# Optimization experiments

Hardware: AMD Instinct MI355X
Metric: run time of the kernel (lower is better)

Reference implementation:

```python
import jax, jax.numpy as jnp
import numpy as np

N_NODES = 100000
N_EDGES = 1600000
D_IN, D_HID, D_OUT = 128, 128, 64


def setup_inputs() -> dict:
    key = jax.random.key(0)
    ks = jax.random.split(key, 8)
    x = jax.random.normal(ks[0], (N_NODES, D_IN), dtype=jnp.float32)
    edge_index = jax.random.randint(ks[1], (2, N_EDGES), 0, N_NODES, dtype=jnp.int64)
    def glorot(k, fan_in, fan_out):
        s = jnp.sqrt(6.0 / (fan_in + fan_out))
        return jax.random.uniform(k, (fan_in, fan_out), jnp.float32, -s, s)
    return {
        "x": x,
        "edge_index": edge_index,
        "W1": glorot(ks[2], D_IN, D_HID), "b1": jnp.zeros((D_HID,), jnp.float32),
        "W2": glorot(ks[3], D_HID, D_HID), "b2": jnp.zeros((D_HID,), jnp.float32),
        "W3": glorot(ks[4], D_HID, D_OUT), "b3": jnp.zeros((D_OUT,), jnp.float32),
    }


def _gcn_norm(edge_index, n_nodes):
    # add self-loops, compute symmetric normalization D^-1/2 A D^-1/2
    loop = jnp.arange(n_nodes, dtype=edge_index.dtype)
    src = jnp.concatenate([edge_index[0], loop])  # message source
    dst = jnp.concatenate([edge_index[1], loop])  # aggregation target
    deg = jax.ops.segment_sum(jnp.ones_like(dst, dtype=jnp.float32), dst,
                              num_segments=n_nodes)
    dinv = jnp.where(deg > 0, jax.lax.rsqrt(deg), 0.0)
    norm = dinv[src] * dinv[dst]  # [E + N]
    return src, dst, norm


def _gcn_conv(x, W, b, src, dst, norm, n_nodes):
    xw = x @ W                                # dense transform [N, F_out]
    msg = xw[src] * norm[:, None]             # gather + scale   [E+N, F_out]
    out = jax.ops.segment_sum(msg, dst, num_segments=n_nodes)  # scatter-add
    return out + b


def reference(x, edge_index, W1, b1, W2, b2, W3, b3):
    n = x.shape[0]
    src, dst, norm = _gcn_norm(edge_index, n)  # cached=True: same norm reused
    h = jax.nn.relu(_gcn_conv(x, W1, b1, src, dst, norm, n))
    h = jax.nn.relu(_gcn_conv(h, W2, b2, src, dst, norm, n))
    return _gcn_conv(h, W3, b3, src, dst, norm, n)
```

## Files before the change

kernel.cpp:

```cpp
#include <hip/hip_runtime.h>
#include <hip/hip_fp16.h>


#define NN 100000
#define NE 1600000
#define TT (NE + NN)
#define BSH 9
#define NBUCK ((NN + 511) / 512)
#define EPB1 2048
#define NPB1 ((TT + EPB1 - 1) / EPB1)

typedef _Float16 f16x8 __attribute__((ext_vector_type(8)));
typedef float f32x4 __attribute__((ext_vector_type(4)));


__global__ __launch_bounds__(256) void wt_conv_all(const float* __restrict__ W1,
                                                   const float* __restrict__ W2,
                                                   const float* __restrict__ W3,
                                                   _Float16* __restrict__ Wt1,
                                                   _Float16* __restrict__ Wt2,
                                                   _Float16* __restrict__ Wt3,
                                                   int* __restrict__ gbc,
                                                   int* __restrict__ done,
                                                   int* __restrict__ bbase,
                                                   int* __restrict__ rowptr) {
    int idx = blockIdx.x * 256 + threadIdx.x;
    if (idx < 16384) {
        Wt1[(idx % 128) * 128 + idx / 128] = (_Float16)W1[idx];
    } else if (idx < 32768) {
        int i = idx - 16384;
        Wt2[(i % 128) * 128 + i / 128] = (_Float16)W2[i];
    } else if (idx < 40960) {
        int i = idx - 32768;
        Wt3[(i % 64) * 128 + i / 64] = (_Float16)W3[i];
    }
    if (idx < NBUCK) gbc[idx] = 0;
    if (idx == 0) { *done = 0; bbase[NBUCK] = TT; rowptr[NN] = TT; }
}


__global__ __launch_bounds__(256) void bucket_count(const int* __restrict__ ei,
                                                    int* __restrict__ gbc,
                                                    int* __restrict__ done,
                                                    int* __restrict__ bbase,
                                                    int* __restrict__ gcursor) {
    __shared__ int hist[NBUCK];
    __shared__ int amlast;
    const int tid = threadIdx.x;
    const int base = blockIdx.x * EPB1;
    for (int b = tid; b < NBUCK; b += 256) hist[b] = 0;
    __syncthreads();
    for (int i = tid; i < EPB1; i += 256) {
        int e = base + i;
        if (e >= TT) break;
        int d = (e < NE) ? ei[NE + e] : (e - NE);
        atomicAdd(&hist[d >> BSH], 1);
    }
    __syncthreads();
    for (int b = tid; b < NBUCK; b += 256)
        if (hist[b]) atomicAdd(&gbc[b], hist[b]);
    __threadfence();
    if (tid == 0) amlast = (atomicAdd(done, 1) == (int)gridDim.x - 1);
    __syncthreads();
    if (amlast) {
        __threadfence();
        __shared__ int s[256];
        int v = (tid < NBUCK)
            ? __hip_atomic_load(&gbc[tid], __ATOMIC_RELAXED,
                                __HIP_MEMORY_SCOPE_AGENT) : 0;
        s[tid] = v;
        __syncthreads();
        for (int off = 1; off < 256; off <<= 1) {
            int u = (tid >= off) ? s[tid - off] : 0;
            __syncthreads();
            s[tid] += u;
            __syncthreads();
        }
        if (tid < NBUCK) {
            int excl = s[tid] - v;
            bbase[tid] = excl;
            gcursor[tid] = excl;
        }
    }
}


__global__ __launch_bounds__(256) void partition_p1(const int* __restrict__ ei,
                                                    int* __restrict__ gcursor,
                                                    int* __restrict__ part) {
    __shared__ int hist[NBUCK];
    const int tid = threadIdx.x;
    const int base = blockIdx.x * EPB1;
    for (int b = tid; b < NBUCK; b += 256) hist[b] = 0;
    __syncthreads();
    for (int i = tid; i < EPB1; i += 256) {
        int e = base + i;
        if (e >= TT) break;
        int d = (e < NE) ? ei[NE + e] : (e - NE);
        atomicAdd(&hist[d >> BSH], 1);
    }
    __syncthreads();
    for (int b = tid; b < NBUCK; b += 256) {
        int cnt = hist[b];
        hist[b] = cnt ? atomicAdd(&gcursor[b], cnt) : 0;
    }
    __syncthreads();
    for (int i = tid; i < EPB1; i += 256) {
        int e = base + i;
        if (e >= TT) break;
        int s, d;
        if (e < NE) { s = ei[e]; d = ei[NE + e]; }
        else        { s = d = e - NE; }
        int pos = atomicAdd(&hist[d >> BSH], 1);
        part[pos] = s | ((d & 511) << 17);
    }
}


__global__ __launch_bounds__(512) void partition_p2(const int* __restrict__ part,
                                                    const int* __restrict__ bbase,
                                                    int* __restrict__ rowptr,
                                                    float* __restrict__ dinv,
                                                    int* __restrict__ col) {
    __shared__ int cnt[512];
    __shared__ int scn[512];
    __shared__ int cur[512];
    const int b = blockIdx.x;
    const int v0 = b << BSH;
    const int nv = min(512, NN - v0);
    const int tid = threadIdx.x;
    const int base = bbase[b];
    const int nrec = bbase[b + 1] - base;

    cnt[tid] = 0;
    __syncthreads();
    for (int i = tid; i < nrec; i += 512)
        atomicAdd(&cnt[((unsigned)part[base + i]) >> 17], 1);
    __syncthreads();
    scn[tid] = cnt[tid];
    __syncthreads();
    for (int off = 1; off < 512; off <<= 1) {
        int a = (tid >= off) ? scn[tid - off] : 0;
        __syncthreads();
        scn[tid] += a;
        __syncthreads();
    }
    if (tid < nv) {
        int excl = scn[tid] - cnt[tid];
        rowptr[v0 + tid] = base + excl;
        dinv[v0 + tid] = rsqrtf((float)cnt[tid]);
        cur[tid] = base + excl;
    }
    __syncthreads();
    for (int i = tid; i < nrec; i += 512) {
        int r = part[base + i];
        int pos = atomicAdd(&cur[((unsigned)r) >> 17], 1);
        col[pos] = r & 0x1FFFF;
    }
}


template <int F, bool AHALF>
__global__ __launch_bounds__(256) void gemm_mfma(const void* __restrict__ Ap,
                                                 const _Float16* __restrict__ Wt,
                                                 const float* __restrict__ dinv,
                                                 __half* __restrict__ Yh) {
    constexpr int NT = F / 16;
    __shared__ _Float16 Yl[64][136];

    const int tid = threadIdx.x;
    const int wave = tid >> 6;
    const int lane = tid & 63;
    const int m = lane & 15;
    const int q = lane >> 4;
    const int grow0 = blockIdx.x * 64;
    const int row = grow0 + wave * 16 + m;
    const bool rok = row < NN;

    f32x4 acc[NT];
#pragma unroll
    for (int t = 0; t < NT; t++) acc[t] = (f32x4){0.f, 0.f, 0.f, 0.f};

#pragma unroll
    for (int kt = 0; kt < 128; kt += 32) {
        const int k0 = kt + q * 8;
        union { f16x8 v; _Float16 e[8]; } au;
        if (rok) {
            if constexpr (AHALF) {
                au.v = *reinterpret_cast<const f16x8*>(
                    (const __half*)Ap + (size_t)row * 128 + k0);
            } else {
                const float* A = (const float*)Ap;
                float4 x0 = *reinterpret_cast<const float4*>(A + (size_t)row * 128 + k0);
                float4 x1 = *reinterpret_cast<const float4*>(A + (size_t)row * 128 + k0 + 4);
                au.e[0] = (_Float16)x0.x; au.e[1] = (_Float16)x0.y;
                au.e[2] = (_Float16)x0.z; au.e[3] = (_Float16)x0.w;
                au.e[4] = (_Float16)x1.x; au.e[5] = (_Float16)x1.y;
                au.e[6] = (_Float16)x1.z; au.e[7] = (_Float16)x1.w;
            }
        } else {
#pragma unroll
            for (int j = 0; j < 8; j++) au.e[j] = (_Float16)0.f;
        }
#pragma unroll
        for (int t = 0; t < NT; t++) {
            f16x8 bf = *reinterpret_cast<const f16x8*>(Wt + (t * 16 + m) * 128 + k0);
            acc[t] = __builtin_amdgcn_mfma_f32_16x16x32_f16(au.v, bf, acc[t], 0, 0, 0);
        }
    }
#pragma unroll
    for (int r = 0; r < 4; r++) {
        int lrow = wave * 16 + q * 4 + r;
        int gr = grow0 + lrow;
        float s = (gr < NN) ? dinv[gr] : 0.f;
#pragma unroll
        for (int t = 0; t < NT; t++)
            Yl[lrow][t * 16 + m] = (_Float16)(s * acc[t][r]);
    }
    __syncthreads();
    constexpr int CH = F / 8;
    for (int i = tid; i < 64 * CH; i += 256) {
        int lrow = i / CH, c = i % CH;
        int gr = grow0 + lrow;
        if (gr < NN)
            *reinterpret_cast<f16x8*>(Yh + (size_t)gr * F + c * 8) =
                *reinterpret_cast<const f16x8*>(&Yl[lrow][c * 8]);
    }
}


__device__ __forceinline__ void acc_add8(float* acc, float4 raw) {
    const __half2* h2 = reinterpret_cast<const __half2*>(&raw);
#pragma unroll
    for (int qq = 0; qq < 4; qq++) {
        float2 fv = __half22float2(h2[qq]);
        acc[2 * qq]     += fv.x;
        acc[2 * qq + 1] += fv.y;
    }
}


template <int FOUT>
__global__ __launch_bounds__(256) void fused_agg_gemm(
        const __half* __restrict__ XWh,
        const int* __restrict__ rowptr,
        const int* __restrict__ col,
        const float* __restrict__ dinv,
        const float* __restrict__ bias,
        const _Float16* __restrict__ Wt,
        __half* __restrict__ Yout) {
    __shared__ _Float16 Hs[16][136];
    __shared__ _Float16 Ds[16][FOUT + 8];

    const int tid = threadIdx.x;
    const int v0 = blockIdx.x * 16;

    {
        const int lnode = tid >> 4;
        const int f = tid & 15;
        const int v = v0 + lnode;
        const int beg = rowptr[v];
        const int end = rowptr[v + 1];
        const float4* base = reinterpret_cast<const float4*>(XWh);
        float acc[8] = {0.f, 0.f, 0.f, 0.f, 0.f, 0.f, 0.f, 0.f};
#pragma unroll 4
        for (int e = beg; e < end; e++) {
            int u = col[e];
            float4 raw = base[(size_t)u * 16 + f];
            acc_add8(acc, raw);
        }
        const float dv = dinv[v];
        union { f16x8 v8; _Float16 e8[8]; } hu;
#pragma unroll
        for (int qq = 0; qq < 8; qq++) {
            float r = dv * acc[qq] + bias[f * 8 + qq];
            hu.e8[qq] = (_Float16)fmaxf(r, 0.f);
        }
        *reinterpret_cast<f16x8*>(&Hs[lnode][f * 8]) = hu.v8;
    }
    __syncthreads();

    constexpr int TPW = FOUT / 64;
    const int wave = tid >> 6;
    const int lane = tid & 63;
    const int m = lane & 15;
    const int q = lane >> 4;
    f32x4 gacc[TPW];
#pragma unroll
    for (int t = 0; t < TPW; t++) gacc[t] = (f32x4){0.f, 0.f, 0.f, 0.f};
#pragma unroll
    for (int kt = 0; kt < 128; kt += 32) {
        const int k0 = kt + q * 8;
        f16x8 av = *reinterpret_cast<const f16x8*>(&Hs[m][k0]);
#pragma unroll
        for (int t = 0; t < TPW; t++) {
            const int gc = (wave * TPW + t) * 16 + m;
            f16x8 bv = *reinterpret_cast<const f16x8*>(Wt + gc * 128 + k0);
            gacc[t] = __builtin_amdgcn_mfma_f32_16x16x32_f16(av, bv, gacc[t], 0, 0, 0);
        }
    }
#pragma unroll
    for (int r = 0; r < 4; r++) {
        const int lrow = q * 4 + r;
        const float s = dinv[v0 + lrow];
#pragma unroll
        for (int t = 0; t < TPW; t++)
            Ds[lrow][(wave * TPW + t) * 16 + m] = (_Float16)(s * gacc[t][r]);
    }
    __syncthreads();
    constexpr int CH = FOUT / 8;
    for (int i2 = tid; i2 < 16 * CH; i2 += 256) {
        int lrow = i2 / CH, c = i2 % CH;
        *reinterpret_cast<f16x8*>(Yout + (size_t)(v0 + lrow) * FOUT + c * 8) =
            *reinterpret_cast<const f16x8*>(&Ds[lrow][c * 8]);
    }
}


__global__ __launch_bounds__(256) void agg_final(
        const __half* __restrict__ XWh,
        const int* __restrict__ rowptr,
        const int* __restrict__ col,
        const float* __restrict__ dinv,
        const float* __restrict__ bias,
        float* __restrict__ out) {
    constexpr int TPN = 8;
    constexpr int NPB = 256 / TPN;
    const int v = blockIdx.x * NPB + threadIdx.x / TPN;
    const int f = threadIdx.x % TPN;
    const int beg = rowptr[v];
    const int end = rowptr[v + 1];
    const float4* base = reinterpret_cast<const float4*>(XWh);
    float acc[8] = {0.f, 0.f, 0.f, 0.f, 0.f, 0.f, 0.f, 0.f};
#pragma unroll 4
    for (int e = beg; e < end; e++) {
        int u = col[e];
        float4 raw = base[(size_t)u * TPN + f];
        acc_add8(acc, raw);
    }
    const float dv = dinv[v];
    float r[8];
#pragma unroll
    for (int q = 0; q < 8; q++)
        r[q] = dv * acc[q] + bias[f * 8 + q];
    float* op = out + (size_t)v * 64 + f * 8;
    *reinterpret_cast<float4*>(op)     = make_float4(r[0], r[1], r[2], r[3]);
    *reinterpret_cast<float4*>(op + 4) = make_float4(r[4], r[5], r[6], r[7]);
}


extern "C" void kernel_launch(void* const* d_in, const int* in_sizes, int n_in,
                              void* d_out, int out_size, void* d_ws, size_t ws_size,
                              hipStream_t stream) {
    const float* x  = (const float*)d_in[0];
    const int*   ei = (const int*)d_in[1];
    const float* W1 = (const float*)d_in[2];
    const float* b1 = (const float*)d_in[3];
    const float* W2 = (const float*)d_in[4];
    const float* b2 = (const float*)d_in[5];
    const float* W3 = (const float*)d_in[6];
    const float* b3 = (const float*)d_in[7];
    float* out = (float*)d_out;

    char* p = (char*)d_ws;
    int*      rowptr  = (int*)p;       p += 400016;
    float*    dinv    = (float*)p;     p += 400000;
    int*      gbc     = (int*)p;       p += 1024;
    int*      bbase   = (int*)p;       p += 1024;
    int*      gcursor = (int*)p;       p += 1024;
    int*      done    = (int*)p;       p += 1024;
    _Float16* Wt1     = (_Float16*)p;  p += 32768;
    _Float16* Wt2     = (_Float16*)p;  p += 32768;
    _Float16* Wt3     = (_Float16*)p;  p += 16384;
    int*      part    = (int*)p;       p += (size_t)TT * 4;
    int*      col     = (int*)p;       p += (size_t)TT * 4;
    __half*   xwh1    = (__half*)p;    p += (size_t)NN * 128 * 2;
    __half*   xwh2    = (__half*)p;
    __half*   xwh3    = xwh1;

    wt_conv_all<<<160, 256, 0, stream>>>(W1, W2, W3, Wt1, Wt2, Wt3,
                                         gbc, done, bbase, rowptr);
    bucket_count<<<NPB1, 256, 0, stream>>>(ei, gbc, done, bbase, gcursor);
    partition_p1<<<NPB1, 256, 0, stream>>>(ei, gcursor, part);
    partition_p2<<<NBUCK, 512, 0, stream>>>(part, bbase, rowptr, dinv, col);

    const int gb = (NN + 63) / 64;
    const int fb = NN / 16;
    gemm_mfma<128, false><<<gb, 256, 0, stream>>>(x, Wt1, dinv, xwh1);
    fused_agg_gemm<128><<<fb, 256, 0, stream>>>(xwh1, rowptr, col, dinv, b1,
                                                Wt2, xwh2);
    fused_agg_gemm<64><<<fb, 256, 0, stream>>>(xwh2, rowptr, col, dinv, b2,
                                               Wt3, xwh3);
    agg_final<<<NN / 32, 256, 0, stream>>>(xwh3, rowptr, col, dinv, b3, out);
}
```

Baseline: 471.4 us.

## Drop bucket-count pass by partitioning into fixed-capacity bucket slots

```diff
diff --git a/kernel.cpp b/kernel.cpp
--- a/kernel.cpp
+++ b/kernel.cpp
@@ -7,8 +7,9 @@
 #define TT (NE + NN)
 #define BSH 9
 #define NBUCK ((NN + 511) / 512)
-#define EPB1 2048
+#define EPB1 8192
 #define NPB1 ((TT + EPB1 - 1) / EPB1)
+#define SLOT 12288
 
 typedef _Float16 f16x8 __attribute__((ext_vector_type(8)));
 typedef float f32x4 __attribute__((ext_vector_type(4)));
@@ -20,9 +21,7 @@
                                                    _Float16* __restrict__ Wt1,
                                                    _Float16* __restrict__ Wt2,
                                                    _Float16* __restrict__ Wt3,
-                                                   int* __restrict__ gbc,
-                                                   int* __restrict__ done,
-                                                   int* __restrict__ bbase,
+                                                   int* __restrict__ gcursor,
                                                    int* __restrict__ rowptr) {
     int idx = blockIdx.x * 256 + threadIdx.x;
     if (idx < 16384) {
@@ -34,109 +33,74 @@
         int i = idx - 32768;
         Wt3[(i % 64) * 128 + i / 64] = (_Float16)W3[i];
     }
-    if (idx < NBUCK) gbc[idx] = 0;
-    if (idx == 0) { *done = 0; bbase[NBUCK] = TT; rowptr[NN] = TT; }
-}
-
-
-__global__ __launch_bounds__(256) void bucket_count(const int* __restrict__ ei,
-                                                    int* __restrict__ gbc,
-                                                    int* __restrict__ done,
-                                                    int* __restrict__ bbase,
-                                                    int* __restrict__ gcursor) {
+    if (idx < NBUCK) gcursor[idx] = 0;
+    if (idx == 0) rowptr[NN] = TT;
+}
+
+
+__global__ __launch_bounds__(1024) void partition_p1(const int* __restrict__ ei,
+                                                     int* __restrict__ gcursor,
+                                                     int* __restrict__ part) {
     __shared__ int hist[NBUCK];
-    __shared__ int amlast;
     const int tid = threadIdx.x;
     const int base = blockIdx.x * EPB1;
-    for (int b = tid; b < NBUCK; b += 256) hist[b] = 0;
-    __syncthreads();
-    for (int i = tid; i < EPB1; i += 256) {
+    for (int b = tid; b < NBUCK; b += 1024) hist[b] = 0;
+    __syncthreads();
+    for (int i = tid; i < EPB1; i += 1024) {
         int e = base + i;
         if (e >= TT) break;
         int d = (e < NE) ? ei[NE + e] : (e - NE);
         atomicAdd(&hist[d >> BSH], 1);
     }
     __syncthreads();
-    for (int b = tid; b < NBUCK; b += 256)
-        if (hist[b]) atomicAdd(&gbc[b], hist[b]);
-    __threadfence();
-    if (tid == 0) amlast = (atomicAdd(done, 1) == (int)gridDim.x - 1);
-    __syncthreads();
-    if (amlast) {
-        __threadfence();
-        __shared__ int s[256];
-        int v = (tid < NBUCK)
-            ? __hip_atomic_load(&gbc[tid], __ATOMIC_RELAXED,
-                                __HIP_MEMORY_SCOPE_AGENT) : 0;
-        s[tid] = v;
-        __syncthreads();
-        for (int off = 1; off < 256; off <<= 1) {
-            int u = (tid >= off) ? s[tid - off] : 0;
-            __syncthreads();
-            s[tid] += u;
-            __syncthreads();
-        }
-        if (tid < NBUCK) {
-            int excl = s[tid] - v;
-            bbase[tid] = excl;
-            gcursor[tid] = excl;
-        }
-    }
-}
-
-
-__global__ __launch_bounds__(256) void partition_p1(const int* __restrict__ ei,
-                                                    int* __restrict__ gcursor,
-                                                    int* __restrict__ part) {
-    __shared__ int hist[NBUCK];
-    const int tid = threadIdx.x;
-    const int base = blockIdx.x * EPB1;
-    for (int b = tid; b < NBUCK; b += 256) hist[b] = 0;
-    __syncthreads();
-    for (int i = tid; i < EPB1; i += 256) {
-        int e = base + i;
-        if (e >= TT) break;
-        int d = (e < NE) ? ei[NE + e] : (e - NE);
-        atomicAdd(&hist[d >> BSH], 1);
-    }
-    __syncthreads();
-    for (int b = tid; b < NBUCK; b += 256) {
+    for (int b = tid; b < NBUCK; b += 1024) {
         int cnt = hist[b];
         hist[b] = cnt ? atomicAdd(&gcursor[b], cnt) : 0;
     }
     __syncthreads();
-    for (int i = tid; i < EPB1; i += 256) {
+    for (int i = tid; i < EPB1; i += 1024) {
         int e = base + i;
         if (e >= TT) break;
         int s, d;
         if (e < NE) { s = ei[e]; d = ei[NE + e]; }
         else        { s = d = e - NE; }
-        int pos = atomicAdd(&hist[d >> BSH], 1);
-        part[pos] = s | ((d & 511) << 17);
+        int bk = d >> BSH;
+        int pos = atomicAdd(&hist[bk], 1);
+        part[bk * SLOT + pos] = s | ((d & 511) << 17);
     }
 }
 
 
 __global__ __launch_bounds__(512) void partition_p2(const int* __restrict__ part,
-                                                    const int* __restrict__ bbase,
+                                                    const int* __restrict__ gcnt,
                                                     int* __restrict__ rowptr,
                                                     float* __restrict__ dinv,
                                                     int* __restrict__ col) {
+    __shared__ int red[512];
     __shared__ int cnt[512];
     __shared__ int scn[512];
     __shared__ int cur[512];
+    __shared__ int sbase;
     const int b = blockIdx.x;
     const int v0 = b << BSH;
     const int nv = min(512, NN - v0);
     const int tid = threadIdx.x;
-    const int base = bbase[b];
-    const int nrec = bbase[b + 1] - base;
-
+    const int nrec = gcnt[b];
+    const int* bp = part + (size_t)b * SLOT;
+
+    red[tid] = (tid < b) ? gcnt[tid] : 0;
     cnt[tid] = 0;
     __syncthreads();
+    for (int off = 256; off > 0; off >>= 1) {
+        if (tid < off) red[tid] += red[tid + off];
+        __syncthreads();
+    }
+    if (tid == 0) sbase = red[0];
+
     for (int i = tid; i < nrec; i += 512)
-        atomicAdd(&cnt[((unsigned)part[base + i]) >> 17], 1);
-    __syncthreads();
+        atomicAdd(&cnt[((unsigned)bp[i]) >> 17], 1);
+    __syncthreads();
+    const int base = sbase;
     scn[tid] = cnt[tid];
     __syncthreads();
     for (int off = 1; off < 512; off <<= 1) {
@@ -153,7 +117,7 @@
     }
     __syncthreads();
     for (int i = tid; i < nrec; i += 512) {
-        int r = part[base + i];
+        int r = bp[i];
         int pos = atomicAdd(&cur[((unsigned)r) >> 17], 1);
         col[pos] = r & 0x1FFFF;
     }
@@ -365,24 +329,20 @@
     char* p = (char*)d_ws;
     int*      rowptr  = (int*)p;       p += 400016;
     float*    dinv    = (float*)p;     p += 400000;
-    int*      gbc     = (int*)p;       p += 1024;
-    int*      bbase   = (int*)p;       p += 1024;
     int*      gcursor = (int*)p;       p += 1024;
-    int*      done    = (int*)p;       p += 1024;
     _Float16* Wt1     = (_Float16*)p;  p += 32768;
     _Float16* Wt2     = (_Float16*)p;  p += 32768;
     _Float16* Wt3     = (_Float16*)p;  p += 16384;
-    int*      part    = (int*)p;       p += (size_t)TT * 4;
+    int*      part    = (int*)p;       p += (size_t)NBUCK * SLOT * 4;
     int*      col     = (int*)p;       p += (size_t)TT * 4;
     __half*   xwh1    = (__half*)p;    p += (size_t)NN * 128 * 2;
     __half*   xwh2    = (__half*)p;
     __half*   xwh3    = xwh1;
 
     wt_conv_all<<<160, 256, 0, stream>>>(W1, W2, W3, Wt1, Wt2, Wt3,
-                                         gbc, done, bbase, rowptr);
-    bucket_count<<<NPB1, 256, 0, stream>>>(ei, gbc, done, bbase, gcursor);
-    partition_p1<<<NPB1, 256, 0, stream>>>(ei, gcursor, part);
-    partition_p2<<<NBUCK, 512, 0, stream>>>(part, bbase, rowptr, dinv, col);
+                                         gcursor, rowptr);
+    partition_p1<<<NPB1, 1024, 0, stream>>>(ei, gcursor, part);
+    partition_p2<<<NBUCK, 512, 0, stream>>>(part, gcursor, rowptr, dinv, col);
 
     const int gb = (NN + 63) / 64;
     const int fb = NN / 16;
```

After: 399.4 us, median of 2. 15.3% less time.
